# Kernel optimization log

Hardware: AMD Instinct MI355X
Metric: run time of the kernel (lower is better)

The kernel has to match this reference:

```python
import jax, jax.numpy as jnp
import numpy as np

MAX_REL = 30
N_HEADS = 8


def conv1d(x, w, b=None, groups=1):
    # x: [B, L, Cin], w: [Cout, Cin/groups, K]  (torch Conv1d layout), 'same' padding
    pad = w.shape[-1] // 2
    y = jax.lax.conv_general_dilated(
        x, w, window_strides=(1,), padding=[(pad, pad)],
        dimension_numbers=("NLC", "OIL", "NLC"), feature_group_count=groups)
    return y if b is None else y + b


def setup_inputs() -> dict:
    key = jax.random.key(0)
    ks = jax.random.split(key, 16)
    B, L, S = 8, 1024, 512          # L = 2 * S (required by Gamma.repeat(1,2,1))
    sd, vd, dm = 512, 64, 512       # spatial_dim == d_model (residual add)
    D = 3 * vd                      # rel-pos / K,V channel dim

    def n(k, shape, s):
        return (jax.random.normal(k, shape, jnp.float32) * s).astype(jnp.float32)

    return {
        "x_spatial": jax.random.normal(ks[0], (B, L, sd), jnp.float32),
        "x_velocity": jax.random.normal(ks[1], (B, S, vd), jnp.float32),
        "w_gamma": n(ks[2], (dm, vd, 1), 0.05)[:, :, 0],      # conv_gamma 1x1, no bias -> [dm, vd]
        "w3": n(ks[3], (vd, vd, 3), 0.07), "b3": jnp.zeros((vd,), jnp.float32),
        "w5": n(ks[4], (vd, vd, 5), 0.05), "b5": jnp.zeros((vd,), jnp.float32),
        "w7": n(ks[5], (vd, vd, 7), 0.04), "b7": jnp.zeros((vd,), jnp.float32),
        "rel_table": n(ks[6], (2 * MAX_REL + 1, D), 0.05),    # embedding [61, 192]
        "dw_w": n(ks[7], (D, 1, 3), 0.3), "dw_b": jnp.zeros((D,), jnp.float32),
        "wq": n(ks[8], (dm, sd), 0.03),
        "wk": n(ks[9], (dm, D), 0.05),
        "wv": n(ks[10], (dm, D), 0.05),
        "fc_w": n(ks[11], (dm, dm), 0.03), "fc_b": jnp.zeros((dm,), jnp.float32),
        "ln_g": jnp.ones((dm,), jnp.float32), "ln_b": jnp.zeros((dm,), jnp.float32),
    }


def rel_pos_enc(ms, rel_table, dw_w, dw_b):
    # Math-equivalent reduction of the torch O(B*S^2*D) op:
    # output[b,j] = mean_i where(i==j, dwconv_row_i(fused)[j], fused[b,i,j])
    #            = ms[b,j] + mean_i rel[i,j] + (diag_conv[b,j] - fused[b,j,j]) / S
    B, S, D = ms.shape
    pos = jnp.arange(S)
    idx = jnp.clip(pos[None, :] - pos[:, None], -MAX_REL, MAX_REL) + MAX_REL  # [S,S]
    mean_rel = rel_table[idx].mean(axis=0)                                    # [S,D]
    # fused[b,i,j] = ms[b,j] + rel_table[idx[i,j]]; diagonal uses idx = MAX_REL,
    # its +/-1 neighbors along j use MAX_REL -/+ ... -> rel[i,i-1]=MAX_REL-1, rel[i,i+1]=MAX_REL+1
    center = ms + rel_table[MAX_REL]                                          # fused[b,i,i]
    left = jnp.pad(ms[:, :-1] + rel_table[MAX_REL - 1], ((0, 0), (1, 0), (0, 0)))   # conv zero-pads at i=0
    right = jnp.pad(ms[:, 1:] + rel_table[MAX_REL + 1], ((0, 0), (0, 1), (0, 0)))   # conv zero-pads at i=S-1
    diag_conv = dw_w[:, 0, 0] * left + dw_w[:, 0, 1] * center + dw_w[:, 0, 2] * right + dw_b
    return ms + mean_rel[None] + (diag_conv - center) / S


def reference(x_spatial, x_velocity, w_gamma, w3, b3, w5, b5, w7, b7,
              rel_table, dw_w, dw_b, wq, wk, wv, fc_w, fc_b, ln_g, ln_b):
    B, S, vd = x_velocity.shape
    _, L, _ = x_spatial.shape
    dm = wq.shape[0]
    dk = dm // N_HEADS

    gamma = jax.nn.sigmoid(jnp.einsum("bsc,dc->bsd", x_velocity, w_gamma))   # [B,S,dm]

    ms = jnp.concatenate([conv1d(x_velocity, w3, b3),
                          conv1d(x_velocity, w5, b5),
                          conv1d(x_velocity, w7, b7)], axis=-1)              # [B,S,3vd]
    x_pe = rel_pos_enc(ms, rel_table, dw_w, dw_b)                            # [B,S,3vd]

    q = jnp.einsum("blc,dc->bld", x_spatial, wq).reshape(B, L, N_HEADS, dk).transpose(0, 2, 1, 3)
    k = jnp.einsum("bsc,dc->bsd", x_pe, wk).reshape(B, S, N_HEADS, dk).transpose(0, 2, 1, 3)
    v = jnp.einsum("bsc,dc->bsd", x_pe, wv).reshape(B, S, N_HEADS, dk).transpose(0, 2, 1, 3)

    scores = jnp.einsum("bhld,bhsd->bhls", q, k) / jnp.sqrt(jnp.float32(dk))
    attn = jax.nn.softmax(scores, axis=-1)                                   # dropout: eval mode (identity)
    out = jnp.einsum("bhls,bhsd->bhld", attn, v)                             # [B,H,L,dk]
    out = out.transpose(0, 2, 1, 3).reshape(B, L, dm)
    out = out @ fc_w.T + fc_b

    out = jnp.tile(gamma, (1, 2, 1)) * out                                   # L == 2*S
    res = x_spatial + out
    mu = res.mean(-1, keepdims=True)
    var = res.var(-1, keepdims=True)
    return (res - mu) / jnp.sqrt(var + 1e-5) * ln_g + ln_b
```

## Files before the change

### kernel.cpp

```cpp
#include <hip/hip_runtime.h>
#include <hip/hip_bf16.h>

constexpr int B  = 8;
constexpr int L  = 1024;
constexpr int S  = 512;
constexpr int VD = 64;
constexpr int DM = 512;
constexpr int D3 = 192;
constexpr int H  = 8;
constexpr int DK = 64;

typedef __attribute__((ext_vector_type(8))) short s8v;
typedef __attribute__((ext_vector_type(4))) float f4v;

__device__ inline unsigned short f2b(float f) {
    unsigned int u = __builtin_bit_cast(unsigned int, f);
    u += 0x7fffu + ((u >> 16) & 1u);
    return (unsigned short)(u >> 16);
}
__device__ inline float b2f(unsigned int lo16) {
    return __builtin_bit_cast(float, lo16 << 16);
}

__device__ __forceinline__ void gload16(const void* g, void* l) {
    __builtin_amdgcn_global_load_lds(
        (const __attribute__((address_space(1))) void*)g,
        (__attribute__((address_space(3))) void*)l, 16, 0, 0);
}

struct CastArgs {
    const float* src[7];
    unsigned short* dst[7];
    int n[7];
    float scale[7];
};

__global__ __launch_bounds__(256) void cast7_k(CastArgs a) {
    int id = blockIdx.y;
    const float* s = a.src[id];
    unsigned short* d = a.dst[id];
    int n = a.n[id];
    float sc = a.scale[id];
    for (long i = (long)(blockIdx.x * 256 + threadIdx.x) * 4; i < n;
         i += (long)gridDim.x * 1024) {
        float4 f = *(const float4*)(s + i);
        ushort4 o;
        o.x = f2b(f.x * sc); o.y = f2b(f.y * sc);
        o.z = f2b(f.z * sc); o.w = f2b(f.w * sc);
        *(ushort4*)(d + i) = o;
    }
}

__global__ __launch_bounds__(192) void prep_k(
    const float* __restrict__ w3, const float* __restrict__ w5,
    const float* __restrict__ w7, const float* __restrict__ dw_w,
    const float* __restrict__ rel_table, const float* __restrict__ b3,
    const float* __restrict__ b5, const float* __restrict__ b7,
    const float* __restrict__ dw_b,
    unsigned short* __restrict__ WpeT, unsigned short* __restrict__ Cp)
{
    int o = threadIdx.x;
    float inv = 1.0f / S;

    if (blockIdx.x < 640) {
        int n = blockIdx.x;
        if (n >= 576) { WpeT[n * D3 + o] = 0; return; }
        int j = n >> 6, c = n & 63, delta = j - 4;
        const float* w; int KW, P, oo;
        if (o < 64)       { w = w3; KW = 3; P = 1; oo = o; }
        else if (o < 128) { w = w5; KW = 5; P = 2; oo = o - 64; }
        else              { w = w7; KW = 7; P = 3; oo = o - 128; }
        float mu0 = dw_w[o * 3 + 0] * inv;
        float mu1 = 1.f + (dw_w[o * 3 + 1] - 1.f) * inv;
        float mu2 = dw_w[o * 3 + 2] * inv;
        float acc = 0.f;
        int k;
        k = delta + 1 + P; if (k >= 0 && k < KW) acc += mu0 * w[(oo * 64 + c) * KW + k];
        k = delta + P;     if (k >= 0 && k < KW) acc += mu1 * w[(oo * 64 + c) * KW + k];
        k = delta - 1 + P; if (k >= 0 && k < KW) acc += mu2 * w[(oo * 64 + c) * KW + k];
        WpeT[n * D3 + o] = f2b(acc);
        return;
    }

    int j = blockIdx.x - 640;
    float acc = 0.f;
#pragma unroll
    for (int r = 1; r < 60; r++) {
        int i = j - (r - 30);
        if (i >= 0 && i < S) acc += rel_table[r * D3 + o];
    }
    float c60 = (float)max(0, j - 29);
    float c0  = (float)max(0, (S - 30) - j);
    acc += c60 * rel_table[60 * D3 + o] + c0 * rel_table[0 * D3 + o];
    float mean_rel = acc * inv;

    float bo  = (o < 64) ? b3[o] : (o < 128) ? b5[o - 64] : b7[o - 128];
    float dw0 = dw_w[o * 3], dw1 = dw_w[o * 3 + 1], dw2 = dw_w[o * 3 + 2];
    float r29 = rel_table[29 * D3 + o], r30 = rel_table[30 * D3 + o],
          r31 = rel_table[31 * D3 + o];
    float alpha = 1.f + (dw1 - 1.f) * inv, beta = dw0 * inv, gamma = dw2 * inv;

    float cp = mean_rel + bo * alpha + (dw1 * r30 + dw_b[o] - r30) * inv;
    if (j > 0)     cp += beta * bo + dw0 * r29 * inv;
    if (j < S - 1) cp += gamma * bo + dw2 * r31 * inv;
    Cp[j * D3 + o] = f2b(cp);
}

__global__ __launch_bounds__(256) void pre_gemm_k(
    const unsigned short* __restrict__ wk_bf,
    const unsigned short* __restrict__ wv_bf,
    const unsigned short* __restrict__ WpeT,
    const unsigned short* __restrict__ Cp,
    unsigned short* __restrict__ WEff,
    unsigned short* __restrict__ Cb)
{
    __shared__ __align__(16) unsigned short As[128 * 64];
    __shared__ __align__(16) unsigned short Bs[128 * 64];

    int z = blockIdx.z;
    const unsigned short* A;
    const unsigned short* Bm;
    unsigned short* C;
    int N, ldc;
    if (z < 2) { A = z ? wv_bf : wk_bf; Bm = WpeT; C = WEff + (long)z * DM * 640; N = 640; ldc = 640; }
    else       { A = Cp; Bm = (z == 2) ? wk_bf : wv_bf; C = Cb + (long)(z - 2) * S * DM; N = 512; ldc = 512; }

    int m0 = blockIdx.x * 128, n0 = blockIdx.y * 128;
    if (n0 >= N) return;

    int t = threadIdx.x;
    int l = t & 63, w = t >> 6;
    int lx = l & 15, lh = l >> 4;
    int wr = w >> 1, wc = w & 1;

    f4v acc[4][4] = {};

    for (int k0 = 0; k0 < D3; k0 += 64) {
        __syncthreads();
#pragma unroll
        for (int p = 0; p < 4; p++) {
            int flat = p * 256 + t;
            int r = flat >> 3, c = flat & 7;
            int csw = (c ^ (r & 7)) * 8;
            gload16(A  + (long)(m0 + r) * D3 + k0 + csw, As + flat * 8);
            gload16(Bm + (long)(n0 + r) * D3 + k0 + csw, Bs + flat * 8);
        }
        __syncthreads();
#pragma unroll
        for (int ks = 0; ks < 2; ks++) {
            s8v af[4], bf[4];
#pragma unroll
            for (int i = 0; i < 4; i++) {
                int ra = wr * 64 + i * 16 + lx;
                af[i] = *(const s8v*)(As + ra * 64 + (((ks * 4 + lh) ^ (ra & 7)) * 8));
                int rb = wc * 64 + i * 16 + lx;
                bf[i] = *(const s8v*)(Bs + rb * 64 + (((ks * 4 + lh) ^ (rb & 7)) * 8));
            }
#pragma unroll
            for (int i = 0; i < 4; i++)
#pragma unroll
                for (int j = 0; j < 4; j++)
                    acc[i][j] = __builtin_amdgcn_mfma_f32_16x16x32_bf16(
                        af[i], bf[j], acc[i][j], 0, 0, 0);
        }
    }

#pragma unroll
    for (int i = 0; i < 4; i++) {
#pragma unroll
        for (int r = 0; r < 4; r++) {
            int m = m0 + wr * 64 + i * 16 + lh * 4 + r;
#pragma unroll
            for (int j = 0; j < 4; j++) {
                int n = n0 + wc * 64 + j * 16 + lx;
                C[(long)m * ldc + n] = f2b(acc[i][j][r]);
            }
        }
    }
}

template<bool BF16OUT>
__global__ __launch_bounds__(256) void gemm_bf16_nt(
    const unsigned short* __restrict__ A, const unsigned short* __restrict__ Bm,
    void* __restrict__ Cout, const float* __restrict__ bias,
    int M, int N, int K, int lda, int ldb, int ldc)
{
    __shared__ __align__(16) unsigned short As[128 * 64];
    __shared__ __align__(16) unsigned short Bs[128 * 64];

    int t = threadIdx.x;
    int l = t & 63, w = t >> 6;
    int lx = l & 15, lh = l >> 4;
    int wr = w >> 1, wc = w & 1;
    int m0 = blockIdx.x * 128, n0 = blockIdx.y * 128;

    f4v acc[4][4] = {};

    for (int k0 = 0; k0 < K; k0 += 64) {
        __syncthreads();
#pragma unroll
        for (int p = 0; p < 4; p++) {
            int flat = p * 256 + t;
            int r = flat >> 3, c = flat & 7;
            int csw = (c ^ (r & 7)) * 8;
            gload16(A  + (long)(m0 + r) * lda + k0 + csw, As + flat * 8);
            gload16(Bm + (long)(n0 + r) * ldb + k0 + csw, Bs + flat * 8);
        }
        __syncthreads();
#pragma unroll
        for (int ks = 0; ks < 2; ks++) {
            s8v af[4], bf[4];
#pragma unroll
            for (int i = 0; i < 4; i++) {
                int ra = wr * 64 + i * 16 + lx;
                af[i] = *(const s8v*)(As + ra * 64 + (((ks * 4 + lh) ^ (ra & 7)) * 8));
                int rb = wc * 64 + i * 16 + lx;
                bf[i] = *(const s8v*)(Bs + rb * 64 + (((ks * 4 + lh) ^ (rb & 7)) * 8));
            }
#pragma unroll
            for (int i = 0; i < 4; i++)
#pragma unroll
                for (int j = 0; j < 4; j++)
                    acc[i][j] = __builtin_amdgcn_mfma_f32_16x16x32_bf16(
                        af[i], bf[j], acc[i][j], 0, 0, 0);
        }
    }

#pragma unroll
    for (int i = 0; i < 4; i++) {
#pragma unroll
        for (int r = 0; r < 4; r++) {
            int m = m0 + wr * 64 + i * 16 + lh * 4 + r;
#pragma unroll
            for (int j = 0; j < 4; j++) {
                int n = n0 + wc * 64 + j * 16 + lx;
                float v = acc[i][j][r];
                if (bias) v += bias[n];
                if (BF16OUT) ((unsigned short*)Cout)[(long)m * ldc + n] = f2b(v);
                else         ((float*)Cout)[(long)m * ldc + n] = v;
            }
        }
    }
}

__global__ __launch_bounds__(256) void convgemm_k(
    const unsigned short* __restrict__ xvb,
    const unsigned short* __restrict__ Weff0,
    const unsigned short* __restrict__ bias0,
    unsigned short* __restrict__ Cout0,
    const unsigned short* __restrict__ zsrc)
{
    __shared__ __align__(16) unsigned short As[128 * 64];
    __shared__ __align__(16) unsigned short Bs[128 * 64];

    int z = blockIdx.z;
    const unsigned short* Weff = Weff0 + (long)z * DM * 640;
    const unsigned short* bias2d = bias0 + (long)z * S * DM;
    unsigned short* Cout = Cout0 + (long)z * B * S * DM;

    int t = threadIdx.x;
    int l = t & 63, w = t >> 6;
    int lx = l & 15, lh = l >> 4;
    int wr = w >> 1, wc = w & 1;
    int m0 = blockIdx.x * 128, n0 = blockIdx.y * 128;
    int b = m0 >> 9, s0 = m0 & 511;

    f4v acc[4][4] = {};

    for (int j = 0; j < 9; j++) {
        __syncthreads();
#pragma unroll
        for (int p = 0; p < 4; p++) {
            int flat = p * 256 + t;
            int r = flat >> 3, c = flat & 7;
            int csw = (c ^ (r & 7)) * 8;
            int ss = s0 + r + j - 4;
            const unsigned short* asrc = (ss >= 0 && ss < S)
                ? xvb + ((long)b * S + ss) * VD + csw : zsrc;
            gload16(asrc, As + flat * 8);
            gload16(Weff + (long)(n0 + r) * 640 + j * 64 + csw, Bs + flat * 8);
        }
        __syncthreads();
#pragma unroll
        for (int ks = 0; ks < 2; ks++) {
            s8v af[4], bf[4];
#pragma unroll
            for (int i = 0; i < 4; i++) {
                int ra = wr * 64 + i * 16 + lx;
                af[i] = *(const s8v*)(As + ra * 64 + (((ks * 4 + lh) ^ (ra & 7)) * 8));
                int rb = wc * 64 + i * 16 + lx;
                bf[i] = *(const s8v*)(Bs + rb * 64 + (((ks * 4 + lh) ^ (rb & 7)) * 8));
            }
#pragma unroll
            for (int i = 0; i < 4; i++)
#pragma unroll
                for (int jj = 0; jj < 4; jj++)
                    acc[i][jj] = __builtin_amdgcn_mfma_f32_16x16x32_bf16(
                        af[i], bf[jj], acc[i][jj], 0, 0, 0);
        }
    }

#pragma unroll
    for (int i = 0; i < 4; i++) {
#pragma unroll
        for (int r = 0; r < 4; r++) {
            int m = m0 + wr * 64 + i * 16 + lh * 4 + r;
            int s = m & 511;
#pragma unroll
            for (int jj = 0; jj < 4; jj++) {
                int n = n0 + wc * 64 + jj * 16 + lx;
                Cout[(long)m * DM + n] =
                    f2b(acc[i][jj][r] + b2f(bias2d[(long)s * DM + n]));
            }
        }
    }
}

__global__ __launch_bounds__(256) void attn_mfma_k(
    const unsigned short* __restrict__ qb, const unsigned short* __restrict__ kb,
    const unsigned short* __restrict__ vb, unsigned short* __restrict__ ob)
{
    __shared__ __align__(16) unsigned short Qs[64 * 64];
    __shared__ __align__(16) unsigned short Ks[64 * 64];
    __shared__ __align__(16) unsigned short Vt[64 * 64];
    __shared__ __align__(16) unsigned short Ps[64 * 64];

    int lt = blockIdx.x, h = blockIdx.y, b = blockIdx.z;
    int t = threadIdx.x, l = t & 63, w = t >> 6, lx = l & 15, lh = l >> 4;

    const unsigned short* qg = qb + ((long)(b * L + lt * 64)) * DM + h * 64;
    const unsigned short* kg = kb + ((long)b * S) * DM + h * 64;
    const unsigned short* vg = vb + ((long)b * S) * DM + h * 64;

#pragma unroll
    for (int p = 0; p < 2; p++) {
        int flat = p * 256 + t;
        int r = flat >> 3, c = flat & 7;
        s8v v = *(const s8v*)(qg + (long)r * DM + c * 8);
        *(s8v*)(Qs + r * 64 + ((c ^ (r & 7)) * 8)) = v;
    }

    int kr0 = t >> 3, kc = t & 7;
    int vs = t & 63, vdq = t >> 6;
    s8v k0, k1, v0, v1;

    auto loadKV = [&](int st) {
        k0 = *(const s8v*)(kg + (long)(st * 64 + kr0) * DM + kc * 8);
        k1 = *(const s8v*)(kg + (long)(st * 64 + 32 + kr0) * DM + kc * 8);
        const unsigned short* vp = vg + (long)(st * 64 + vs) * DM + vdq * 16;
        v0 = *(const s8v*)(vp);
        v1 = *(const s8v*)(vp + 8);
    };
    auto writeKV = [&]() {
        *(s8v*)(Ks + kr0 * 64 + ((kc ^ (kr0 & 7)) * 8)) = k0;
        int r2 = 32 + kr0;
        *(s8v*)(Ks + r2 * 64 + ((kc ^ (r2 & 7)) * 8)) = k1;
#pragma unroll
        for (int e = 0; e < 8; e++) {
            int d1 = vdq * 16 + e;
            Vt[d1 * 64 + (((vs >> 3) ^ (d1 & 7)) * 8) + (vs & 7)] =
                (unsigned short)v0[e];
            int d2 = vdq * 16 + 8 + e;
            Vt[d2 * 64 + (((vs >> 3) ^ (d2 & 7)) * 8) + (vs & 7)] =
                (unsigned short)v1[e];
        }
    };

    loadKV(0);
    writeKV();
    __syncthreads();

    float lrow[4] = {0.f, 0.f, 0.f, 0.f};
    f4v oacc[4] = {};

    for (int st = 0; st < S / 64; st++) {
        if (st < S / 64 - 1) loadKV(st + 1);

        f4v pacc[4] = {};
        __builtin_amdgcn_s_setprio(1);
#pragma unroll
        for (int ks = 0; ks < 2; ks++) {
            int qr = w * 16 + lx;
            s8v a = *(const s8v*)(Qs + qr * 64 + (((ks * 4 + lh) ^ (qr & 7)) * 8));
#pragma unroll
            for (int jf = 0; jf < 4; jf++) {
                int kr = jf * 16 + lx;
                s8v bf = *(const s8v*)(Ks + kr * 64 + (((ks * 4 + lh) ^ (kr & 7)) * 8));
                pacc[jf] = __builtin_amdgcn_mfma_f32_16x16x32_bf16(a, bf, pacc[jf], 0, 0, 0);
            }
        }
        __builtin_amdgcn_s_setprio(0);

#pragma unroll
        for (int r = 0; r < 4; r++) {
            int prow = w * 16 + lh * 4 + r;
#pragma unroll
            for (int jf = 0; jf < 4; jf++) {
                float pe = __builtin_amdgcn_exp2f(pacc[jf][r]);
                lrow[r] += pe;
                int col = jf * 16 + lx;
                Ps[prow * 64 + (((col >> 3) ^ (prow & 7)) * 8) + (col & 7)] = f2b(pe);
            }
        }
        asm volatile("s_waitcnt lgkmcnt(0)" ::: "memory");

        __builtin_amdgcn_s_setprio(1);
#pragma unroll
        for (int ks2 = 0; ks2 < 2; ks2++) {
            int pr = w * 16 + lx;
            s8v pa = *(const s8v*)(Ps + pr * 64 + (((ks2 * 4 + lh) ^ (pr & 7)) * 8));
#pragma unroll
            for (int df = 0; df < 4; df++) {
                int vr = df * 16 + lx;
                s8v vf = *(const s8v*)(Vt + vr * 64 + (((ks2 * 4 + lh) ^ (vr & 7)) * 8));
                oacc[df] = __builtin_amdgcn_mfma_f32_16x16x32_bf16(pa, vf, oacc[df], 0, 0, 0);
            }
        }
        __builtin_amdgcn_s_setprio(0);
        __syncthreads();
        if (st < S / 64 - 1) {
            writeKV();
            __syncthreads();
        }
    }

    unsigned short* og = ob + ((long)(b * L + lt * 64 + w * 16)) * DM + h * 64;
#pragma unroll
    for (int r = 0; r < 4; r++) {
        float ls = lrow[r];
#pragma unroll
        for (int msk = 1; msk < 16; msk <<= 1) ls += __shfl_xor(ls, msk);
        float inv = 1.f / ls;
#pragma unroll
        for (int df = 0; df < 4; df++)
            og[(long)(lh * 4 + r) * DM + df * 16 + lx] = f2b(oacc[df][r] * inv);
    }
}

__global__ __launch_bounds__(256) void final_k(
    const float* __restrict__ xs, const unsigned short* __restrict__ fcb,
    const unsigned short* __restrict__ gb,
    const float* __restrict__ ln_g, const float* __restrict__ ln_b,
    float* __restrict__ out)
{
    int bl = blockIdx.x;
    int b = bl >> 10, lq = bl & 1023;
    int t = threadIdx.x;
    int d0 = t * 2;
    const unsigned short* g = gb + ((long)b * S + (lq & 511)) * DM;

    __shared__ float red[2][4];

    float2 xv = *(const float2*)(xs + (long)bl * DM + d0);
    unsigned int fp = *(const unsigned int*)(fcb + (long)bl * DM + d0);
    unsigned int gp = *(const unsigned int*)(g + d0);

    float fo0 = b2f(fp & 0xffffu), fo1 = b2f(fp >> 16);
    float ga0 = 1.f / (1.f + __expf(-b2f(gp & 0xffffu)));
    float ga1 = 1.f / (1.f + __expf(-b2f(gp >> 16)));
    float r0 = xv.x + ga0 * fo0;
    float r1 = xv.y + ga1 * fo1;

    float sum = r0 + r1, sumsq = r0 * r0 + r1 * r1;
#pragma unroll
    for (int msk = 1; msk < 64; msk <<= 1) {
        sum   += __shfl_xor(sum, msk);
        sumsq += __shfl_xor(sumsq, msk);
    }
    int wave = t >> 6;
    if ((t & 63) == 0) { red[0][wave] = sum; red[1][wave] = sumsq; }
    __syncthreads();
    float tot   = red[0][0] + red[0][1] + red[0][2] + red[0][3];
    float totsq = red[1][0] + red[1][1] + red[1][2] + red[1][3];

    float mu  = tot * (1.0f / DM);
    float var = totsq * (1.0f / DM) - mu * mu;
    float inv = rsqrtf(var + 1e-5f);

    float2 lg = *(const float2*)(ln_g + d0);
    float2 lb = *(const float2*)(ln_b + d0);
    float2 o;
    o.x = (r0 - mu) * inv * lg.x + lb.x;
    o.y = (r1 - mu) * inv * lg.y + lb.y;
    *(float2*)(out + (long)bl * DM + d0) = o;
}

extern "C" void kernel_launch(void* const* d_in, const int* in_sizes, int n_in,
                              void* d_out, int out_size, void* d_ws, size_t ws_size,
                              hipStream_t stream) {
    (void)in_sizes; (void)n_in; (void)out_size; (void)ws_size;

    const float* x_spatial  = (const float*)d_in[0];
    const float* x_velocity = (const float*)d_in[1];
    const float* w_gamma    = (const float*)d_in[2];
    const float* w3 = (const float*)d_in[3];
    const float* b3 = (const float*)d_in[4];
    const float* w5 = (const float*)d_in[5];
    const float* b5 = (const float*)d_in[6];
    const float* w7 = (const float*)d_in[7];
    const float* b7 = (const float*)d_in[8];
    const float* rel_table = (const float*)d_in[9];
    const float* dw_w = (const float*)d_in[10];
    const float* dw_b = (const float*)d_in[11];
    const float* wq   = (const float*)d_in[12];
    const float* wk   = (const float*)d_in[13];
    const float* wv   = (const float*)d_in[14];
    const float* fc_w = (const float*)d_in[15];
    const float* fc_b = (const float*)d_in[16];
    const float* ln_g = (const float*)d_in[17];
    const float* ln_b = (const float*)d_in[18];
    float* out = (float*)d_out;

    char* p = (char*)d_ws;
    auto alloc = [&](size_t bytes) {
        char* r = p;
        p += (bytes + 255) & ~(size_t)255;
        return r;
    };
    unsigned short* gamma_bf = (unsigned short*)alloc((size_t)B * S * DM * 2);
    unsigned short* fcb      = (unsigned short*)alloc((size_t)B * L * DM * 2);
    unsigned short* xs_bf   = (unsigned short*)alloc((size_t)B * L * DM * 2);
    unsigned short* xv_bf   = (unsigned short*)alloc((size_t)B * S * VD * 2);
    unsigned short* qbuf    = (unsigned short*)alloc((size_t)B * L * DM * 2);
    unsigned short* kbuf    = (unsigned short*)alloc((size_t)B * S * DM * 2);
    unsigned short* vbuf    = (unsigned short*)alloc((size_t)B * S * DM * 2);
    unsigned short* attn_bf = (unsigned short*)alloc((size_t)B * L * DM * 2);
    unsigned short* wq_bf   = (unsigned short*)alloc((size_t)DM * DM * 2);
    unsigned short* wk_bf   = (unsigned short*)alloc((size_t)DM * D3 * 2);
    unsigned short* wv_bf   = (unsigned short*)alloc((size_t)DM * D3 * 2);
    unsigned short* fcw_bf  = (unsigned short*)alloc((size_t)DM * DM * 2);
    unsigned short* wg_bf   = (unsigned short*)alloc((size_t)DM * VD * 2);
    unsigned short* WpeT    = (unsigned short*)alloc((size_t)640 * D3 * 2);
    unsigned short* Cp      = (unsigned short*)alloc((size_t)S * D3 * 2);
    unsigned short* WkEff   = (unsigned short*)alloc((size_t)DM * 640 * 2);
    unsigned short* WvEff   = (unsigned short*)alloc((size_t)DM * 640 * 2);
    unsigned short* Ckb     = (unsigned short*)alloc((size_t)S * DM * 2);
    unsigned short* Cvb     = (unsigned short*)alloc((size_t)S * DM * 2);
    (void)WvEff; (void)Cvb;

    CastArgs ca;
    ca.src[0] = x_spatial;  ca.dst[0] = xs_bf;  ca.n[0] = B * L * DM; ca.scale[0] = 1.f;
    ca.src[1] = x_velocity; ca.dst[1] = xv_bf;  ca.n[1] = B * S * VD; ca.scale[1] = 1.f;
    ca.src[2] = wq;         ca.dst[2] = wq_bf;  ca.n[2] = DM * DM;    ca.scale[2] = 0.125f * 1.44269504089f;
    ca.src[3] = wk;         ca.dst[3] = wk_bf;  ca.n[3] = DM * D3;    ca.scale[3] = 1.f;
    ca.src[4] = wv;         ca.dst[4] = wv_bf;  ca.n[4] = DM * D3;    ca.scale[4] = 1.f;
    ca.src[5] = fc_w;       ca.dst[5] = fcw_bf; ca.n[5] = DM * DM;    ca.scale[5] = 1.f;
    ca.src[6] = w_gamma;    ca.dst[6] = wg_bf;  ca.n[6] = DM * VD;    ca.scale[6] = 1.f;
    cast7_k<<<dim3(1024, 7), 256, 0, stream>>>(ca);

    prep_k<<<dim3(1152), 192, 0, stream>>>(
        w3, w5, w7, dw_w, rel_table, b3, b5, b7, dw_b, WpeT, Cp);

    pre_gemm_k<<<dim3(4, 5, 4), 256, 0, stream>>>(
        wk_bf, wv_bf, WpeT, Cp, WkEff, Ckb);

    gemm_bf16_nt<true><<<dim3(32, 4), 256, 0, stream>>>(
        xv_bf, wg_bf, gamma_bf, nullptr, B * S, DM, VD, VD, VD, DM);

    gemm_bf16_nt<true><<<dim3(64, 4), 256, 0, stream>>>(
        xs_bf, wq_bf, qbuf, nullptr, B * L, DM, DM, DM, DM, DM);

    convgemm_k<<<dim3(32, 4, 2), 256, 0, stream>>>(
        xv_bf, WkEff, Ckb, kbuf, WkEff + 576 );

    attn_mfma_k<<<dim3(L / 64, H, B), 256, 0, stream>>>(qbuf, kbuf, vbuf, attn_bf);

    gemm_bf16_nt<true><<<dim3(64, 4), 256, 0, stream>>>(
        attn_bf, fcw_bf, fcb, fc_b, B * L, DM, DM, DM, DM, DM);

    final_k<<<dim3(B * L), 256, 0, stream>>>(
        x_spatial, fcb, gamma_bf, ln_g, ln_b, out);
}
```

Measured before the change: 210.3 us.

## Merge independent prep, small GEMM and Q/conv kernels into fewer launches

Merges the cast and prep kernels into one launch using a second grid dimension. Folds the gamma GEMM into the pre-GEMM kernel, and runs the Q projection GEMM in the same launch as the conv-GEMM that produces K/V. The aim is to cut launch count (from 8 to 6) and the idle gaps between small kernels, so independent work shares the GPU. In exchange the grids are padded, many blocks exit early, and the merged kernels may use more registers.

Measured after the change: 188.9 us. 10.2% less time.

```diff
diff --git a/kernel.cpp b/kernel.cpp
--- a/kernel.cpp
+++ b/kernel.cpp
@@ -35,23 +35,8 @@
     float scale[7];
 };
 
-__global__ __launch_bounds__(256) void cast7_k(CastArgs a) {
-    int id = blockIdx.y;
-    const float* s = a.src[id];
-    unsigned short* d = a.dst[id];
-    int n = a.n[id];
-    float sc = a.scale[id];
-    for (long i = (long)(blockIdx.x * 256 + threadIdx.x) * 4; i < n;
-         i += (long)gridDim.x * 1024) {
-        float4 f = *(const float4*)(s + i);
-        ushort4 o;
-        o.x = f2b(f.x * sc); o.y = f2b(f.y * sc);
-        o.z = f2b(f.z * sc); o.w = f2b(f.w * sc);
-        *(ushort4*)(d + i) = o;
-    }
-}
-
-__global__ __launch_bounds__(192) void prep_k(
+__global__ __launch_bounds__(256) void prep_cast_k(
+    CastArgs a,
     const float* __restrict__ w3, const float* __restrict__ w5,
     const float* __restrict__ w7, const float* __restrict__ dw_w,
     const float* __restrict__ rel_table, const float* __restrict__ b3,
@@ -59,7 +44,27 @@
     const float* __restrict__ dw_b,
     unsigned short* __restrict__ WpeT, unsigned short* __restrict__ Cp)
 {
-    int o = threadIdx.x;
+    int t = threadIdx.x;
+    int y = blockIdx.y;
+
+    if (y < 7) {
+        const float* s = a.src[y];
+        unsigned short* d = a.dst[y];
+        int n = a.n[y];
+        float sc = a.scale[y];
+        for (long i = (long)(blockIdx.x * 256 + t) * 4; i < n;
+             i += (long)gridDim.x * 1024) {
+            float4 f = *(const float4*)(s + i);
+            ushort4 o;
+            o.x = f2b(f.x * sc); o.y = f2b(f.y * sc);
+            o.z = f2b(f.z * sc); o.w = f2b(f.w * sc);
+            *(ushort4*)(d + i) = o;
+        }
+        return;
+    }
+
+    if (t >= 192) return;
+    int o = t;
     float inv = 1.0f / S;
 
     if (blockIdx.x < 640) {
@@ -106,93 +111,43 @@
     Cp[j * D3 + o] = f2b(cp);
 }
 
-__global__ __launch_bounds__(256) void pre_gemm_k(
+__global__ __launch_bounds__(256) void pre_gemm5_k(
     const unsigned short* __restrict__ wk_bf,
     const unsigned short* __restrict__ wv_bf,
     const unsigned short* __restrict__ WpeT,
     const unsigned short* __restrict__ Cp,
+    const unsigned short* __restrict__ xv_bf,
+    const unsigned short* __restrict__ wg_bf,
     unsigned short* __restrict__ WEff,
-    unsigned short* __restrict__ Cb)
+    unsigned short* __restrict__ Cb,
+    unsigned short* __restrict__ gamma_bf)
 {
+    int z = blockIdx.z, mx = blockIdx.x, ny = blockIdx.y;
+    const unsigned short *A, *Bm;
+    unsigned short* C;
+    int K, lda, ldb, ldc;
+    if (z < 2) {
+        if (mx >= 4) return;
+        A = z ? wv_bf : wk_bf; Bm = WpeT; C = WEff + (long)z * DM * 640;
+        K = D3; lda = D3; ldb = D3; ldc = 640;
+    } else if (z < 4) {
+        if (mx >= 4 || ny >= 4) return;
+        A = Cp; Bm = (z == 2) ? wk_bf : wv_bf; C = Cb + (long)(z - 2) * S * DM;
+        K = D3; lda = D3; ldb = D3; ldc = DM;
+    } else {
+        if (ny >= 4) return;
+        A = xv_bf; Bm = wg_bf; C = gamma_bf;
+        K = VD; lda = VD; ldb = VD; ldc = DM;
+    }
+
     __shared__ __align__(16) unsigned short As[128 * 64];
     __shared__ __align__(16) unsigned short Bs[128 * 64];
-
-    int z = blockIdx.z;
-    const unsigned short* A;
-    const unsigned short* Bm;
-    unsigned short* C;
-    int N, ldc;
-    if (z < 2) { A = z ? wv_bf : wk_bf; Bm = WpeT; C = WEff + (long)z * DM * 640; N = 640; ldc = 640; }
-    else       { A = Cp; Bm = (z == 2) ? wk_bf : wv_bf; C = Cb + (long)(z - 2) * S * DM; N = 512; ldc = 512; }
-
-    int m0 = blockIdx.x * 128, n0 = blockIdx.y * 128;
-    if (n0 >= N) return;
 
     int t = threadIdx.x;
     int l = t & 63, w = t >> 6;
     int lx = l & 15, lh = l >> 4;
     int wr = w >> 1, wc = w & 1;
-
-    f4v acc[4][4] = {};
-
-    for (int k0 = 0; k0 < D3; k0 += 64) {
-        __syncthreads();
-#pragma unroll
-        for (int p = 0; p < 4; p++) {
-            int flat = p * 256 + t;
-            int r = flat >> 3, c = flat & 7;
-            int csw = (c ^ (r & 7)) * 8;
-            gload16(A  + (long)(m0 + r) * D3 + k0 + csw, As + flat * 8);
-            gload16(Bm + (long)(n0 + r) * D3 + k0 + csw, Bs + flat * 8);
-        }
-        __syncthreads();
-#pragma unroll
-        for (int ks = 0; ks < 2; ks++) {
-            s8v af[4], bf[4];
-#pragma unroll
-            for (int i = 0; i < 4; i++) {
-                int ra = wr * 64 + i * 16 + lx;
-                af[i] = *(const s8v*)(As + ra * 64 + (((ks * 4 + lh) ^ (ra & 7)) * 8));
-                int rb = wc * 64 + i * 16 + lx;
-                bf[i] = *(const s8v*)(Bs + rb * 64 + (((ks * 4 + lh) ^ (rb & 7)) * 8));
-            }
-#pragma unroll
-            for (int i = 0; i < 4; i++)
-#pragma unroll
-                for (int j = 0; j < 4; j++)
-                    acc[i][j] = __builtin_amdgcn_mfma_f32_16x16x32_bf16(
-                        af[i], bf[j], acc[i][j], 0, 0, 0);
-        }
-    }
-
-#pragma unroll
-    for (int i = 0; i < 4; i++) {
-#pragma unroll
-        for (int r = 0; r < 4; r++) {
-            int m = m0 + wr * 64 + i * 16 + lh * 4 + r;
-#pragma unroll
-            for (int j = 0; j < 4; j++) {
-                int n = n0 + wc * 64 + j * 16 + lx;
-                C[(long)m * ldc + n] = f2b(acc[i][j][r]);
-            }
-        }
-    }
-}
-
-template<bool BF16OUT>
-__global__ __launch_bounds__(256) void gemm_bf16_nt(
-    const unsigned short* __restrict__ A, const unsigned short* __restrict__ Bm,
-    void* __restrict__ Cout, const float* __restrict__ bias,
-    int M, int N, int K, int lda, int ldb, int ldc)
-{
-    __shared__ __align__(16) unsigned short As[128 * 64];
-    __shared__ __align__(16) unsigned short Bs[128 * 64];
-
-    int t = threadIdx.x;
-    int l = t & 63, w = t >> 6;
-    int lx = l & 15, lh = l >> 4;
-    int wr = w >> 1, wc = w & 1;
-    int m0 = blockIdx.x * 128, n0 = blockIdx.y * 128;
+    int m0 = mx * 128, n0 = ny * 128;
 
     f4v acc[4][4] = {};
 
@@ -234,16 +189,16 @@
 #pragma unroll
             for (int j = 0; j < 4; j++) {
                 int n = n0 + wc * 64 + j * 16 + lx;
-                float v = acc[i][j][r];
-                if (bias) v += bias[n];
-                if (BF16OUT) ((unsigned short*)Cout)[(long)m * ldc + n] = f2b(v);
-                else         ((float*)Cout)[(long)m * ldc + n] = v;
-            }
-        }
-    }
-}
-
-__global__ __launch_bounds__(256) void convgemm_k(
+                C[(long)m * ldc + n] = f2b(acc[i][j][r]);
+            }
+        }
+    }
+}
+
+__global__ __launch_bounds__(256) void qconv_k(
+    const unsigned short* __restrict__ xs_bf,
+    const unsigned short* __restrict__ wq_bf,
+    unsigned short* __restrict__ qbuf,
     const unsigned short* __restrict__ xvb,
     const unsigned short* __restrict__ Weff0,
     const unsigned short* __restrict__ bias0,
@@ -253,19 +208,68 @@
     __shared__ __align__(16) unsigned short As[128 * 64];
     __shared__ __align__(16) unsigned short Bs[128 * 64];
 
-    int z = blockIdx.z;
-    const unsigned short* Weff = Weff0 + (long)z * DM * 640;
-    const unsigned short* bias2d = bias0 + (long)z * S * DM;
-    unsigned short* Cout = Cout0 + (long)z * B * S * DM;
-
+    int zt = blockIdx.z;
     int t = threadIdx.x;
     int l = t & 63, w = t >> 6;
     int lx = l & 15, lh = l >> 4;
     int wr = w >> 1, wc = w & 1;
+
+    f4v acc[4][4] = {};
+
+    if (zt == 0) {
+        int m0 = blockIdx.x * 128, n0 = blockIdx.y * 128;
+        for (int k0 = 0; k0 < DM; k0 += 64) {
+            __syncthreads();
+#pragma unroll
+            for (int p = 0; p < 4; p++) {
+                int flat = p * 256 + t;
+                int r = flat >> 3, c = flat & 7;
+                int csw = (c ^ (r & 7)) * 8;
+                gload16(xs_bf + (long)(m0 + r) * DM + k0 + csw, As + flat * 8);
+                gload16(wq_bf + (long)(n0 + r) * DM + k0 + csw, Bs + flat * 8);
+            }
+            __syncthreads();
+#pragma unroll
+            for (int ks = 0; ks < 2; ks++) {
+                s8v af[4], bf[4];
+#pragma unroll
+                for (int i = 0; i < 4; i++) {
+                    int ra = wr * 64 + i * 16 + lx;
+                    af[i] = *(const s8v*)(As + ra * 64 + (((ks * 4 + lh) ^ (ra & 7)) * 8));
+                    int rb = wc * 64 + i * 16 + lx;
+                    bf[i] = *(const s8v*)(Bs + rb * 64 + (((ks * 4 + lh) ^ (rb & 7)) * 8));
+                }
+#pragma unroll
+                for (int i = 0; i < 4; i++)
+#pragma unroll
+                    for (int j = 0; j < 4; j++)
+                        acc[i][j] = __builtin_amdgcn_mfma_f32_16x16x32_bf16(
+                            af[i], bf[j], acc[i][j], 0, 0, 0);
+            }
+        }
+#pragma unroll
+        for (int i = 0; i < 4; i++) {
+#pragma unroll
+            for (int r = 0; r < 4; r++) {
+                int m = m0 + wr * 64 + i * 16 + lh * 4 + r;
+#pragma unroll
+                for (int j = 0; j < 4; j++) {
+                    int n = n0 + wc * 64 + j * 16 + lx;
+                    qbuf[(long)m * DM + n] = f2b(acc[i][j][r]);
+                }
+            }
+        }
+        return;
+    }
+
+    if (blockIdx.x >= 32) return;
+    int z = zt - 1;
+    const unsigned short* Weff = Weff0 + (long)z * DM * 640;
+    const unsigned short* bias2d = bias0 + (long)z * S * DM;
+    unsigned short* Cout = Cout0 + (long)z * B * S * DM;
+
     int m0 = blockIdx.x * 128, n0 = blockIdx.y * 128;
     int b = m0 >> 9, s0 = m0 & 511;
-
-    f4v acc[4][4] = {};
 
     for (int j = 0; j < 9; j++) {
         __syncthreads();
@@ -311,6 +315,65 @@
                 int n = n0 + wc * 64 + jj * 16 + lx;
                 Cout[(long)m * DM + n] =
                     f2b(acc[i][jj][r] + b2f(bias2d[(long)s * DM + n]));
+            }
+        }
+    }
+}
+
+__global__ __launch_bounds__(256) void gemm_fc_k(
+    const unsigned short* __restrict__ A, const unsigned short* __restrict__ Bm,
+    unsigned short* __restrict__ Cout, const float* __restrict__ bias)
+{
+    __shared__ __align__(16) unsigned short As[128 * 64];
+    __shared__ __align__(16) unsigned short Bs[128 * 64];
+
+    int t = threadIdx.x;
+    int l = t & 63, w = t >> 6;
+    int lx = l & 15, lh = l >> 4;
+    int wr = w >> 1, wc = w & 1;
+    int m0 = blockIdx.x * 128, n0 = blockIdx.y * 128;
+
+    f4v acc[4][4] = {};
+
+    for (int k0 = 0; k0 < DM; k0 += 64) {
+        __syncthreads();
+#pragma unroll
+        for (int p = 0; p < 4; p++) {
+            int flat = p * 256 + t;
+            int r = flat >> 3, c = flat & 7;
+            int csw = (c ^ (r & 7)) * 8;
+            gload16(A  + (long)(m0 + r) * DM + k0 + csw, As + flat * 8);
+            gload16(Bm + (long)(n0 + r) * DM + k0 + csw, Bs + flat * 8);
+        }
+        __syncthreads();
+#pragma unroll
+        for (int ks = 0; ks < 2; ks++) {
+            s8v af[4], bf[4];
+#pragma unroll
+            for (int i = 0; i < 4; i++) {
+                int ra = wr * 64 + i * 16 + lx;
+                af[i] = *(const s8v*)(As + ra * 64 + (((ks * 4 + lh) ^ (ra & 7)) * 8));
+                int rb = wc * 64 + i * 16 + lx;
+                bf[i] = *(const s8v*)(Bs + rb * 64 + (((ks * 4 + lh) ^ (rb & 7)) * 8));
+            }
+#pragma unroll
+            for (int i = 0; i < 4; i++)
+#pragma unroll
+                for (int j = 0; j < 4; j++)
+                    acc[i][j] = __builtin_amdgcn_mfma_f32_16x16x32_bf16(
+                        af[i], bf[j], acc[i][j], 0, 0, 0);
+        }
+    }
+
+#pragma unroll
+    for (int i = 0; i < 4; i++) {
+#pragma unroll
+        for (int r = 0; r < 4; r++) {
+            int m = m0 + wr * 64 + i * 16 + lh * 4 + r;
+#pragma unroll
+            for (int j = 0; j < 4; j++) {
+                int n = n0 + wc * 64 + j * 16 + lx;
+                Cout[(long)m * DM + n] = f2b(acc[i][j][r] + bias[n]);
             }
         }
     }
@@ -536,7 +599,7 @@
     unsigned short* WvEff   = (unsigned short*)alloc((size_t)DM * 640 * 2);
     unsigned short* Ckb     = (unsigned short*)alloc((size_t)S * DM * 2);
     unsigned short* Cvb     = (unsigned short*)alloc((size_t)S * DM * 2);
-    (void)WvEff; (void)Cvb;
+    (void)wv_bf; (void)WvEff; (void)Cvb;
 
     CastArgs ca;
     ca.src[0] = x_spatial;  ca.dst[0] = xs_bf;  ca.n[0] = B * L * DM; ca.scale[0] = 1.f;
@@ -546,27 +609,19 @@
     ca.src[4] = wv;         ca.dst[4] = wv_bf;  ca.n[4] = DM * D3;    ca.scale[4] = 1.f;
     ca.src[5] = fc_w;       ca.dst[5] = fcw_bf; ca.n[5] = DM * DM;    ca.scale[5] = 1.f;
     ca.src[6] = w_gamma;    ca.dst[6] = wg_bf;  ca.n[6] = DM * VD;    ca.scale[6] = 1.f;
-    cast7_k<<<dim3(1024, 7), 256, 0, stream>>>(ca);
-
-    prep_k<<<dim3(1152), 192, 0, stream>>>(
-        w3, w5, w7, dw_w, rel_table, b3, b5, b7, dw_b, WpeT, Cp);
-
-    pre_gemm_k<<<dim3(4, 5, 4), 256, 0, stream>>>(
-        wk_bf, wv_bf, WpeT, Cp, WkEff, Ckb);
-
-    gemm_bf16_nt<true><<<dim3(32, 4), 256, 0, stream>>>(
-        xv_bf, wg_bf, gamma_bf, nullptr, B * S, DM, VD, VD, VD, DM);
-
-    gemm_bf16_nt<true><<<dim3(64, 4), 256, 0, stream>>>(
-        xs_bf, wq_bf, qbuf, nullptr, B * L, DM, DM, DM, DM, DM);
-
-    convgemm_k<<<dim3(32, 4, 2), 256, 0, stream>>>(
-        xv_bf, WkEff, Ckb, kbuf, WkEff + 576 );
+    prep_cast_k<<<dim3(1152, 8), 256, 0, stream>>>(
+        ca, w3, w5, w7, dw_w, rel_table, b3, b5, b7, dw_b, WpeT, Cp);
+
+    pre_gemm5_k<<<dim3(32, 5, 5), 256, 0, stream>>>(
+        wk_bf, wv_bf, WpeT, Cp, xv_bf, wg_bf, WkEff, Ckb, gamma_bf);
+
+    qconv_k<<<dim3(64, 4, 3), 256, 0, stream>>>(
+        xs_bf, wq_bf, qbuf, xv_bf, WkEff, Ckb, kbuf,
+        WkEff + 576 );
 
     attn_mfma_k<<<dim3(L / 64, H, B), 256, 0, stream>>>(qbuf, kbuf, vbuf, attn_bf);
 
-    gemm_bf16_nt<true><<<dim3(64, 4), 256, 0, stream>>>(
-        attn_bf, fcw_bf, fcb, fc_b, B * L, DM, DM, DM, DM, DM);
+    gemm_fc_k<<<dim3(64, 4), 256, 0, stream>>>(attn_bf, fcw_bf, fcb, fc_b);
 
     final_k<<<dim3(B * L), 256, 0, stream>>>(
         x_spatial, fcb, gamma_bf, ln_g, ln_b, out);
```
